# Kernel tuning notes

Hardware: AMD Instinct MI355X
Metric: run time of the kernel (lower is better)

The kernel has to match this reference:

```python
import jax, jax.numpy as jnp
import numpy as np

B, S, H, D, HID = 1024, 64, 32, 32, 1024
COMP = 256          # smolgen compress_size
TOK = 32            # smolgen token_compress out dim
LN_EPS = 1e-5


def _xavier(key, shape):
    fan_in, fan_out = shape[0], shape[-1]
    std = np.sqrt(2.0 / (fan_in + fan_out))
    return jax.random.normal(key, shape, dtype=jnp.float32) * std


def setup_inputs() -> dict:
    key = jax.random.key(0)
    ks = jax.random.split(key, 12)
    x = jax.random.normal(ks[0], (B, S, HID), dtype=jnp.float32)
    # attention projections (stored [in, out], no bias on qkv)
    Wq = _xavier(ks[1], (HID, H * D))
    Wk = _xavier(ks[2], (HID, H * D))
    Wv = _xavier(ks[3], (HID, H * D))
    Wo = _xavier(ks[4], (H * D, HID))
    bo = jnp.zeros((HID,), dtype=jnp.float32)
    pos_bias = jnp.zeros((H, S, S), dtype=jnp.float32)
    # smolgen params
    tc_W = _xavier(ks[5], (HID, TOK))                  # token_compress, no bias
    pc_W = _xavier(ks[6], (S * TOK, COMP))             # position_compress linear
    pc_b = jnp.zeros((COMP,), dtype=jnp.float32)
    ln_g = jnp.ones((COMP,), dtype=jnp.float32)        # LayerNorm gamma
    ln_b = jnp.zeros((COMP,), dtype=jnp.float32)       # LayerNorm beta
    hp_W = jax.vmap(lambda k: _xavier(k, (COMP, COMP)))(jax.random.split(ks[7], H))  # [H,COMP,COMP]
    hp_b = jnp.zeros((H, COMP), dtype=jnp.float32)
    alp_W = _xavier(ks[8], (COMP, S * S))              # attention_logits_proj
    alp_b = jnp.zeros((S * S,), dtype=jnp.float32)
    return dict(x=x, Wq=Wq, Wk=Wk, Wv=Wv, Wo=Wo, bo=bo, pos_bias=pos_bias,
                tc_W=tc_W, pc_W=pc_W, pc_b=pc_b, ln_g=ln_g, ln_b=ln_b,
                hp_W=hp_W, hp_b=hp_b, alp_W=alp_W, alp_b=alp_b)


def _smolgen(x, tc_W, pc_W, pc_b, ln_g, ln_b, hp_W, hp_b, alp_W, alp_b):
    b = x.shape[0]
    flat = (x @ tc_W).reshape(b, S * TOK)              # [B, 64*32]
    pv = jax.nn.relu(flat @ pc_W + pc_b)               # [B, COMP]
    mu = jnp.mean(pv, axis=-1, keepdims=True)
    var = jnp.mean(jnp.square(pv - mu), axis=-1, keepdims=True)
    pv = (pv - mu) * jax.lax.rsqrt(var + LN_EPS) * ln_g + ln_b
    # per-head projections, vectorized over heads
    hv = jnp.einsum('bc,hcd->bhd', pv, hp_W) + hp_b    # [B, H, COMP]
    logits = jnp.einsum('bhd,de->bhe', hv, alp_W) + alp_b
    return logits.reshape(b, H, S, S)


def reference(x, Wq, Wk, Wv, Wo, bo, pos_bias, tc_W, pc_W, pc_b, ln_g, ln_b,
              hp_W, hp_b, alp_W, alp_b):
    b = x.shape[0]
    scale = 1.0 / np.sqrt(D)
    q = (x @ Wq).reshape(b, S, H, D).transpose(0, 2, 1, 3)  # [B,H,S,D]
    k = (x @ Wk).reshape(b, S, H, D).transpose(0, 2, 1, 3)
    v = (x @ Wv).reshape(b, S, H, D).transpose(0, 2, 1, 3)
    scores = jnp.einsum('bhqd,bhkd->bhqk', q, k) * scale
    scores = scores + pos_bias[None]
    scores = scores + _smolgen(x, tc_W, pc_W, pc_b, ln_g, ln_b, hp_W, hp_b, alp_W, alp_b)
    attn = jax.nn.softmax(scores, axis=-1)
    out = jnp.einsum('bhqk,bhkd->bhqd', attn, v)             # [B,H,S,D]
    out = out.transpose(0, 2, 1, 3).reshape(b, S, H * D)
    return out @ Wo + bo
```

## Files before the change

### kernel.cpp

```cpp
#include <hip/hip_runtime.h>
#include <hip/hip_bf16.h>
#include <cstdint>
#include <cstddef>

typedef __attribute__((ext_vector_type(4))) float f32x4;
typedef __attribute__((ext_vector_type(8))) short short8;
typedef unsigned short u16;
typedef __attribute__((ext_vector_type(8))) unsigned short u16x8;
typedef __attribute__((ext_vector_type(4))) unsigned short u16x4;

__device__ __forceinline__ u16 f2bf(float f) {
  union { float f; unsigned u; } v; v.f = f;
  unsigned r = v.u + 0x7FFFu + ((v.u >> 16) & 1u);
  return (u16)(r >> 16);
}
__device__ __forceinline__ float bf2f(u16 h) {
  union { unsigned u; float f; } v; v.u = ((unsigned)h) << 16;
  return v.f;
}
__device__ __forceinline__ void gload16(const u16* g, const u16* l) {
  __builtin_amdgcn_global_load_lds((const __attribute__((address_space(1))) void*)g,
                                   (__attribute__((address_space(3))) void*)l, 16, 0, 0);
}
__device__ __forceinline__ void fenced_barrier() {
  __builtin_amdgcn_sched_barrier(0);
  __builtin_amdgcn_s_barrier();
  __builtin_amdgcn_sched_barrier(0);
}

__global__ __launch_bounds__(256) void prep_w2t(
    const float* __restrict__ Wq, const float* __restrict__ Wk, const float* __restrict__ Wv,
    const float* __restrict__ tc, u16* __restrict__ W2t)
{
  __shared__ float t[32][33];
  const int tx = threadIdx.x, ty = threadIdx.y;
  const int k0 = blockIdx.x * 32, n0 = blockIdx.y * 32;
  const float* src = nullptr; int col = 0, sw = 0;
  if      (n0 < 1024) { src = Wq; col = n0;        sw = 1024; }
  else if (n0 < 2048) { src = Wk; col = n0 - 1024; sw = 1024; }
  else if (n0 < 3072) { src = Wv; col = n0 - 2048; sw = 1024; }
  else if (n0 < 3104) { src = tc; col = n0 - 3072; sw = 32;   }
  if (src) {
    #pragma unroll
    for (int r = 0; r < 4; r++) {
      int k = k0 + ty + r * 8;
      t[ty + r * 8][tx] = src[(size_t)k * sw + col + tx];
    }
  }
  __syncthreads();
  #pragma unroll
  for (int r = 0; r < 4; r++) {
    int n = n0 + ty + r * 8, k = k0 + tx;
    u16 v = src ? f2bf(t[tx][ty + r * 8]) : (u16)0;
    W2t[(size_t)n * 1024 + k] = v;
  }
}

__global__ __launch_bounds__(256) void transpose_bf(
    const float* __restrict__ src, u16* __restrict__ dst, int R, int C)
{
  __shared__ float t[32][33];
  const int tx = threadIdx.x, ty = threadIdx.y;
  const size_t zoff = (size_t)blockIdx.z * R * C;
  src += zoff; dst += zoff;
  const int c0 = blockIdx.x * 32, r0 = blockIdx.y * 32;
  #pragma unroll
  for (int r = 0; r < 4; r++)
    t[ty + r * 8][tx] = src[(size_t)(r0 + ty + r * 8) * C + c0 + tx];
  __syncthreads();
  #pragma unroll
  for (int r = 0; r < 4; r++)
    dst[(size_t)(c0 + ty + r * 8) * R + r0 + tx] = f2bf(t[tx][ty + r * 8]);
}

__global__ __launch_bounds__(256) void cvt_x(const float* __restrict__ x, u16* __restrict__ A2)
{
  size_t i = (size_t)blockIdx.x * 256 + threadIdx.x;
  f32x4 v = ((const f32x4*)x)[i];
  u16x4 o;
  #pragma unroll
  for (int j = 0; j < 4; j++) o[j] = f2bf(v[j]);
  ((u16x4*)A2)[i] = o;
}

template<int MODE>
__global__ __launch_bounds__(256, 2) void gemm_p(
    const u16* __restrict__ A, const u16* __restrict__ Bt, int K,
    void* __restrict__ o0, void* __restrict__ o1, void* __restrict__ o2, void* __restrict__ o3,
    const float* __restrict__ bias0, const float* __restrict__ bias1)
{
  __shared__ __align__(16) u16 lds[3][12288];
  const int tid = threadIdx.x;
  const int wid = tid >> 6, lane = tid & 63;
  const int wm = wid >> 1, wn = wid & 1;
  const int g = lane >> 4, l15 = lane & 15;

  const int GX = gridDim.x;
  const int nwg = GX * (int)gridDim.y;
  const int lin = (int)blockIdx.y * GX + (int)blockIdx.x;
  const int swz = (lin & 7) * (nwg >> 3) + (lin >> 3);
  const int bn = swz % GX, bm = swz / GX;

  const int lR = lane >> 3;
  const int logi = (lane & 7) ^ lR;
  const int shb = logi >> 2;
  const int sg = logi & 3;

  const u16* pA[4];
  #pragma unroll
  for (int i = 0; i < 4; i++)
    pA[i] = A + (size_t)(bm * 256 + shb * 128 + (wid * 4 + i) * 8 + lR) * K + sg * 8;
  const u16* pB[2];
  #pragma unroll
  for (int i = 0; i < 2; i++)
    pB[i] = Bt + (size_t)(bn * 128 + shb * 64 + (wid * 2 + i) * 8 + lR) * K + sg * 8;

  const int aRd = l15 * 64 + ((((wm << 2) | g) ^ (l15 & 7)) << 3);
  const int bRd = 8192 + l15 * 64 + ((((wn << 2) | g) ^ (l15 & 7)) << 3);

  f32x4 acc[8][4];
  #pragma unroll
  for (int i = 0; i < 8; i++)
    #pragma unroll
    for (int j = 0; j < 4; j++)
      #pragma unroll
      for (int r = 0; r < 4; r++) acc[i][j][r] = 0.f;

  const int NT = K >> 5;

#define STG_A(buf, kt) do {                                              \
    _Pragma("unroll")                                                    \
    for (int i_ = 0; i_ < 4; i_++)                                       \
      gload16(pA[i_] + (size_t)(kt) * 32, &lds[buf][(wid * 4 + i_) * 512]); } while (0)
#define STG_B(buf, kt) do {                                              \
    _Pragma("unroll")                                                    \
    for (int i_ = 0; i_ < 2; i_++)                                       \
      gload16(pB[i_] + (size_t)(kt) * 32, &lds[buf][8192 + (wid * 2 + i_) * 512]); } while (0)

  STG_A(0, 0); STG_B(0, 0);
  STG_A(1, 1); STG_B(1, 1);

  for (int t = 0; t < NT; t++) {
    const int rb = t % 3;
    const int wb = (t + 2) % 3;
    const bool more = (t + 2) < NT;

    if (t + 1 < NT) asm volatile("s_waitcnt vmcnt(6)" ::: "memory");
    else            asm volatile("s_waitcnt vmcnt(0)" ::: "memory");
    fenced_barrier();

    short8 af[8], bfr[4];
    #pragma unroll
    for (int f = 0; f < 4; f++) af[f] = *(const short8*)&lds[rb][aRd + f * 1024];
    #pragma unroll
    for (int n = 0; n < 4; n++) bfr[n] = *(const short8*)&lds[rb][bRd + n * 1024];
    if (more) STG_A(wb, t + 2);
    asm volatile("s_waitcnt lgkmcnt(0)" ::: "memory");
    __builtin_amdgcn_sched_barrier(0);
    __builtin_amdgcn_s_setprio(1);
    #pragma unroll
    for (int f = 0; f < 4; f++)
      #pragma unroll
      for (int n = 0; n < 4; n++)
        acc[f][n] = __builtin_amdgcn_mfma_f32_16x16x32_bf16(af[f], bfr[n], acc[f][n], 0, 0, 0);
    __builtin_amdgcn_s_setprio(0);

    #pragma unroll
    for (int f = 4; f < 8; f++) af[f] = *(const short8*)&lds[rb][aRd + f * 1024];
    if (more) STG_B(wb, t + 2);
    asm volatile("s_waitcnt lgkmcnt(0)" ::: "memory");
    __builtin_amdgcn_sched_barrier(0);
    __builtin_amdgcn_s_setprio(1);
    #pragma unroll
    for (int f = 4; f < 8; f++)
      #pragma unroll
      for (int n = 0; n < 4; n++)
        acc[f][n] = __builtin_amdgcn_mfma_f32_16x16x32_bf16(af[f], bfr[n], acc[f][n], 0, 0, 0);
    __builtin_amdgcn_s_setprio(0);
  }
#undef STG_A
#undef STG_B

  const int lr = lane >> 4, lc = lane & 15;
  #pragma unroll
  for (int fm = 0; fm < 8; fm++) {
    #pragma unroll
    for (int fn = 0; fn < 4; fn++) {
      #pragma unroll
      for (int r = 0; r < 4; r++) {
        int gm = bm * 256 + wm * 128 + fm * 16 + lr * 4 + r;
        int gn = bn * 128 + wn * 64 + fn * 16 + lc;
        float val = acc[fm][fn][r];
        if (MODE == 0) {
          int b = gm >> 6, s = gm & 63;
          if (gn < 3072) {
            int which = gn >> 10, hh = (gn >> 5) & 31, d = gn & 31;
            u16* dst = (which == 0) ? (u16*)o0 : (which == 1) ? (u16*)o1 : (u16*)o2;
            dst[(((size_t)b * 32 + hh) * 64 + s) * 32 + d] = f2bf(val);
          } else if (gn < 3104) {
            ((u16*)o3)[(size_t)b * 2048 + s * 32 + (gn - 3072)] = f2bf(val);
          }
        } else if (MODE == 3) {
          ((u16*)o0)[(size_t)gm * 4096 + gn] = f2bf(val + bias0[gn] + bias1[(gm & 31) * 4096 + gn]);
        } else {
          ((float*)o0)[(size_t)gm * 1024 + gn] = val + bias0[gn];
        }
      }
    }
  }
}

template<int MODE>
__global__ __launch_bounds__(256) void gemm_bt(
    const u16* __restrict__ A, const u16* __restrict__ Bt, int K,
    void* __restrict__ o0, const float* __restrict__ bias0)
{
  __shared__ __align__(16) u16 lA[128 * 32];
  __shared__ __align__(16) u16 lB[128 * 32];
  const int tid = threadIdx.x;
  const int wid = tid >> 6, lane = tid & 63;
  const int wm = wid >> 1, wn = wid & 1;
  const int bn = blockIdx.x, bm = blockIdx.y;
  if (MODE == 2) Bt += (size_t)blockIdx.z * 256 * 256;

  f32x4 acc[4][4];
  #pragma unroll
  for (int i = 0; i < 4; i++)
    #pragma unroll
    for (int j = 0; j < 4; j++)
      #pragma unroll
      for (int r = 0; r < 4; r++) acc[i][j][r] = 0.f;

  const u16* Arow = A + (size_t)(bm * 128) * K;
  const u16* Brow = Bt + (size_t)(bn * 128) * K;

  for (int k0 = 0; k0 < K; k0 += 32) {
    #pragma unroll
    for (int i = 0; i < 2; i++) {
      int c = wid * 128 + i * 64 + lane;
      int row = c >> 2, col = (c & 3) * 8;
      gload16(Arow + (size_t)row * K + k0 + col, &lA[(wid * 128 + i * 64) * 8]);
      gload16(Brow + (size_t)row * K + k0 + col, &lB[(wid * 128 + i * 64) * 8]);
    }
    __syncthreads();
    short8 af[4], bfr[4];
    #pragma unroll
    for (int f = 0; f < 4; f++) {
      af[f]  = *(const short8*)&lA[(wm * 64 + f * 16 + (lane & 15)) * 32 + (lane >> 4) * 8];
      bfr[f] = *(const short8*)&lB[(wn * 64 + f * 16 + (lane & 15)) * 32 + (lane >> 4) * 8];
    }
    #pragma unroll
    for (int fm = 0; fm < 4; fm++)
      #pragma unroll
      for (int fn = 0; fn < 4; fn++)
        acc[fm][fn] = __builtin_amdgcn_mfma_f32_16x16x32_bf16(af[fm], bfr[fn], acc[fm][fn], 0, 0, 0);
    __syncthreads();
  }

  const int lr = lane >> 4, lc = lane & 15;
  #pragma unroll
  for (int fm = 0; fm < 4; fm++) {
    #pragma unroll
    for (int fn = 0; fn < 4; fn++) {
      #pragma unroll
      for (int r = 0; r < 4; r++) {
        int gm = bm * 128 + wm * 64 + fm * 16 + lr * 4 + r;
        int gn = bn * 128 + wn * 64 + fn * 16 + lc;
        float val = acc[fm][fn][r];
        if (MODE == 1) {
          float v = val + bias0[gn];
          ((float*)o0)[(size_t)gm * 256 + gn] = v > 0.f ? v : 0.f;
        } else if (MODE == 2) {
          int h = blockIdx.z;
          ((u16*)o0)[((size_t)gm * 32 + h) * 256 + gn] = f2bf(val + bias0[h * 256 + gn]);
        }
      }
    }
  }
}

__global__ __launch_bounds__(256) void ln_kernel(
    const float* __restrict__ pv, const float* __restrict__ g, const float* __restrict__ b2,
    u16* __restrict__ out)
{
  __shared__ float red[256];
  const int bi = blockIdx.x, t = threadIdx.x;
  float v = pv[(size_t)bi * 256 + t];
  red[t] = v; __syncthreads();
  #pragma unroll
  for (int o = 128; o > 0; o >>= 1) { if (t < o) red[t] += red[t + o]; __syncthreads(); }
  float mu = red[0] * (1.f / 256.f);
  __syncthreads();
  float dv = v - mu;
  red[t] = dv * dv; __syncthreads();
  #pragma unroll
  for (int o = 128; o > 0; o >>= 1) { if (t < o) red[t] += red[t + o]; __syncthreads(); }
  float var = red[0] * (1.f / 256.f);
  float rs = rsqrtf(var + 1e-5f);
  out[(size_t)bi * 256 + t] = f2bf(dv * rs * g[t] + b2[t]);
}

__global__ __launch_bounds__(64) void attn_mfma(
    const u16* __restrict__ qb, const u16* __restrict__ kb, const u16* __restrict__ vb,
    const u16* __restrict__ lg, u16* __restrict__ aout)
{
  __shared__ __align__(16) u16 vT[32 * 64];
  __shared__ __align__(16) u16 Pl[64 * 64];
  const int bid = blockIdx.x;
  const int lane = threadIdx.x;
  const int g = lane >> 4, l15 = lane & 15;
  const size_t base = (size_t)bid * 2048;

  {
    const u16* vrow = vb + base + lane * 32;
    u16x8 vv[4];
    #pragma unroll
    for (int c = 0; c < 4; c++) vv[c] = *(const u16x8*)(vrow + c * 8);
    #pragma unroll
    for (int d = 0; d < 32; d++)
      vT[d * 64 + (lane ^ ((d & 7) << 3))] = vv[d >> 3][d & 7];
  }

  short8 qf[4], kf[4];
  #pragma unroll
  for (int t = 0; t < 4; t++) {
    qf[t] = *(const short8*)(qb + base + (size_t)(t * 16 + l15) * 32 + g * 8);
    kf[t] = *(const short8*)(kb + base + (size_t)(t * 16 + l15) * 32 + g * 8);
  }

  f32x4 s[4][4];
  #pragma unroll
  for (int tm = 0; tm < 4; tm++)
    #pragma unroll
    for (int tn = 0; tn < 4; tn++)
      #pragma unroll
      for (int r = 0; r < 4; r++) s[tm][tn][r] = 0.f;
  #pragma unroll
  for (int tm = 0; tm < 4; tm++)
    #pragma unroll
    for (int tn = 0; tn < 4; tn++)
      s[tm][tn] = __builtin_amdgcn_mfma_f32_16x16x32_bf16(kf[tm], qf[tn], s[tm][tn], 0, 0, 0);

  const float scale = 0.17677669529663687f;
  float inv4[4];
  const u16* lbase = lg + (size_t)bid * 4096;
  #pragma unroll
  for (int tn = 0; tn < 4; tn++) {
    const int q = tn * 16 + l15;
    float mx = -1e30f;
    #pragma unroll
    for (int tm = 0; tm < 4; tm++) {
      u16x4 u = *(const u16x4*)(lbase + (size_t)q * 64 + tm * 16 + g * 4);
      #pragma unroll
      for (int r = 0; r < 4; r++) {
        s[tm][tn][r] = s[tm][tn][r] * scale + bf2f(u[r]);
        mx = fmaxf(mx, s[tm][tn][r]);
      }
    }
    mx = fmaxf(mx, __shfl_xor(mx, 16));
    mx = fmaxf(mx, __shfl_xor(mx, 32));
    float sm = 0.f;
    #pragma unroll
    for (int tm = 0; tm < 4; tm++)
      #pragma unroll
      for (int r = 0; r < 4; r++) {
        float e = __expf(s[tm][tn][r] - mx);
        s[tm][tn][r] = e;
        sm += e;
      }
    sm += __shfl_xor(sm, 16);
    sm += __shfl_xor(sm, 32);
    inv4[tn] = 1.f / sm;
    #pragma unroll
    for (int tm = 0; tm < 4; tm++) {
      u16x4 p;
      #pragma unroll
      for (int r = 0; r < 4; r++) p[r] = f2bf(s[tm][tn][r]);
      *(u16x4*)&Pl[q * 64 + ((tm * 16 + g * 4) ^ ((q & 7) << 3))] = p;
    }
  }
  __syncthreads();

  f32x4 o[2][4];
  #pragma unroll
  for (int md = 0; md < 2; md++)
    #pragma unroll
    for (int tn = 0; tn < 4; tn++)
      #pragma unroll
      for (int r = 0; r < 4; r++) o[md][tn][r] = 0.f;
  #pragma unroll
  for (int ks = 0; ks < 2; ks++) {
    short8 vf2[2], pf[4];
    #pragma unroll
    for (int md = 0; md < 2; md++)
      vf2[md] = *(const short8*)&vT[(md * 16 + l15) * 64 + ((ks * 32 + g * 8) ^ ((l15 & 7) << 3))];
    #pragma unroll
    for (int tn = 0; tn < 4; tn++)
      pf[tn] = *(const short8*)&Pl[(tn * 16 + l15) * 64 + ((ks * 32 + g * 8) ^ ((l15 & 7) << 3))];
    #pragma unroll
    for (int md = 0; md < 2; md++)
      #pragma unroll
      for (int tn = 0; tn < 4; tn++)
        o[md][tn] = __builtin_amdgcn_mfma_f32_16x16x32_bf16(vf2[md], pf[tn], o[md][tn], 0, 0, 0);
  }

  const int b = bid >> 5, h = bid & 31;
  #pragma unroll
  for (int md = 0; md < 2; md++) {
    #pragma unroll
    for (int tn = 0; tn < 4; tn++) {
      const int q = tn * 16 + l15, d0 = md * 16 + g * 4;
      u16x4 u;
      #pragma unroll
      for (int r = 0; r < 4; r++) u[r] = f2bf(o[md][tn][r] * inv4[tn]);
      *(u16x4*)(aout + ((size_t)(b * 64 + q)) * 1024 + h * 32 + d0) = u;
    }
  }
}

extern "C" void kernel_launch(void* const* d_in, const int* in_sizes, int n_in,
                              void* d_out, int out_size, void* d_ws, size_t ws_size,
                              hipStream_t stream) {
  const float* x       = (const float*)d_in[0];
  const float* Wq      = (const float*)d_in[1];
  const float* Wk      = (const float*)d_in[2];
  const float* Wv      = (const float*)d_in[3];
  const float* Wo      = (const float*)d_in[4];
  const float* bo      = (const float*)d_in[5];
  const float* pos_b   = (const float*)d_in[6];
  const float* tc_W    = (const float*)d_in[7];
  const float* pc_W    = (const float*)d_in[8];
  const float* pc_b    = (const float*)d_in[9];
  const float* ln_g    = (const float*)d_in[10];
  const float* ln_b    = (const float*)d_in[11];
  const float* hp_W    = (const float*)d_in[12];
  const float* hp_b    = (const float*)d_in[13];
  const float* alp_W   = (const float*)d_in[14];
  const float* alp_b   = (const float*)d_in[15];
  float* out = (float*)d_out;

  char* w = (char*)d_ws;
  u16* A2     = (u16*)w;
  u16* logits = (u16*)w;              w += 268435456;
  u16* qb     = (u16*)w;              w += 134217728;
  u16* kb     = (u16*)w;              w += 134217728;
  u16* vb     = (u16*)w;              w += 134217728;
  u16* aout   = (u16*)w;              w += 134217728;
  u16* W2t    = (u16*)w;              w += (size_t)3328 * 1024 * 2;
  u16* pcWt   = (u16*)w;              w += (size_t)256 * 2048 * 2;
  u16* hpWt   = (u16*)w;              w += (size_t)32 * 256 * 256 * 2;
  u16* alpWt  = (u16*)w;              w += (size_t)4096 * 256 * 2;
  u16* WoT    = (u16*)w;              w += (size_t)1024 * 1024 * 2;
  u16* flatb  = (u16*)w;              w += (size_t)1024 * 2048 * 2;
  float* pvtmp= (float*)w;            w += (size_t)1024 * 256 * 4;
  u16* pvb    = (u16*)w;              w += (size_t)1024 * 256 * 2;
  u16* hvb    = (u16*)w;              w += (size_t)32768 * 256 * 2;

  prep_w2t    <<<dim3(32, 104),    dim3(32, 8), 0, stream>>>(Wq, Wk, Wv, tc_W, W2t);
  transpose_bf<<<dim3(8, 64, 1),   dim3(32, 8), 0, stream>>>(pc_W, pcWt, 2048, 256);
  transpose_bf<<<dim3(8, 8, 32),   dim3(32, 8), 0, stream>>>(hp_W, hpWt, 256, 256);
  transpose_bf<<<dim3(128, 8, 1),  dim3(32, 8), 0, stream>>>(alp_W, alpWt, 256, 4096);
  transpose_bf<<<dim3(32, 32, 1),  dim3(32, 8), 0, stream>>>(Wo, WoT, 1024, 1024);
  cvt_x       <<<65536, 256, 0, stream>>>(x, A2);

  gemm_p<0> <<<dim3(26, 256),    256, 0, stream>>>(A2, W2t, 1024, qb, kb, vb, flatb, nullptr, nullptr);
  gemm_bt<1><<<dim3(2, 8),       256, 0, stream>>>(flatb, pcWt, 2048, pvtmp, pc_b);
  ln_kernel <<<1024, 256, 0, stream>>>(pvtmp, ln_g, ln_b, pvb);
  gemm_bt<2><<<dim3(2, 8, 32),   256, 0, stream>>>(pvb, hpWt, 256, hvb, hp_b);
  gemm_p<3> <<<dim3(32, 128),    256, 0, stream>>>(hvb, alpWt, 256, logits, nullptr, nullptr, nullptr, alp_b, pos_b);
  attn_mfma <<<32768, 64, 0, stream>>>(qb, kb, vb, logits, aout);
  gemm_p<4> <<<dim3(8, 256),     256, 0, stream>>>(aout, WoT, 1024, out, nullptr, nullptr, nullptr, bo, nullptr);
}
```

Before: 1.085 ms.

## Split gemm_p tile across 8 waves with 512 threads per block

The 256x128 GEMM tile is now computed by 8 waves (512 threads) instead of 4. Each wave owns a 64x64 sub-tile with a 4x4 accumulator array instead of 8x4. Staging drops to three global-to-LDS loads per thread, and the per-iteration work becomes a single MFMA phase. The aim is lower register pressure and more resident waves to hide latency, at the cost of less MFMA work per wave between barriers and more barrier participants.

```diff
diff --git a/kernel.cpp b/kernel.cpp
--- a/kernel.cpp
+++ b/kernel.cpp
@@ -84,7 +84,7 @@
 }
 
 template<int MODE>
-__global__ __launch_bounds__(256, 2) void gemm_p(
+__global__ __launch_bounds__(512, 4) void gemm_p(
     const u16* __restrict__ A, const u16* __restrict__ Bt, int K,
     void* __restrict__ o0, void* __restrict__ o1, void* __restrict__ o2, void* __restrict__ o3,
     const float* __restrict__ bias0, const float* __restrict__ bias1)
@@ -106,21 +106,16 @@
   const int shb = logi >> 2;
   const int sg = logi & 3;
 
-  const u16* pA[4];
+  const u16* pA0 = A + (size_t)(bm * 256 + shb * 128 + (wid * 2 + 0) * 8 + lR) * K + sg * 8;
+  const u16* pA1 = A + (size_t)(bm * 256 + shb * 128 + (wid * 2 + 1) * 8 + lR) * K + sg * 8;
+  const u16* pB  = Bt + (size_t)(bn * 128 + shb * 64 + wid * 8 + lR) * K + sg * 8;
+
+  const int aRd = ((wm & 1) * 64 + l15) * 64 + ((((wm >> 1) << 2) | g) ^ (l15 & 7)) * 8;
+  const int bRd = 8192 + l15 * 64 + ((((wn << 2) | g) ^ (l15 & 7)) * 8);
+
+  f32x4 acc[4][4];
   #pragma unroll
   for (int i = 0; i < 4; i++)
-    pA[i] = A + (size_t)(bm * 256 + shb * 128 + (wid * 4 + i) * 8 + lR) * K + sg * 8;
-  const u16* pB[2];
-  #pragma unroll
-  for (int i = 0; i < 2; i++)
-    pB[i] = Bt + (size_t)(bn * 128 + shb * 64 + (wid * 2 + i) * 8 + lR) * K + sg * 8;
-
-  const int aRd = l15 * 64 + ((((wm << 2) | g) ^ (l15 & 7)) << 3);
-  const int bRd = 8192 + l15 * 64 + ((((wn << 2) | g) ^ (l15 & 7)) << 3);
-
-  f32x4 acc[8][4];
-  #pragma unroll
-  for (int i = 0; i < 8; i++)
     #pragma unroll
     for (int j = 0; j < 4; j++)
       #pragma unroll
@@ -128,33 +123,28 @@
 
   const int NT = K >> 5;
 
-#define STG_A(buf, kt) do {                                              \
-    _Pragma("unroll")                                                    \
-    for (int i_ = 0; i_ < 4; i_++)                                       \
-      gload16(pA[i_] + (size_t)(kt) * 32, &lds[buf][(wid * 4 + i_) * 512]); } while (0)
-#define STG_B(buf, kt) do {                                              \
-    _Pragma("unroll")                                                    \
-    for (int i_ = 0; i_ < 2; i_++)                                       \
-      gload16(pB[i_] + (size_t)(kt) * 32, &lds[buf][8192 + (wid * 2 + i_) * 512]); } while (0)
-
-  STG_A(0, 0); STG_B(0, 0);
-  STG_A(1, 1); STG_B(1, 1);
+#define STG(buf, kt) do {                                                   \
+    gload16(pA0 + (size_t)(kt) * 32, &lds[buf][(wid * 2 + 0) * 512]);       \
+    gload16(pA1 + (size_t)(kt) * 32, &lds[buf][(wid * 2 + 1) * 512]);       \
+    gload16(pB  + (size_t)(kt) * 32, &lds[buf][8192 + wid * 512]); } while (0)
+
+  STG(0, 0); STG(1, 1);
 
   for (int t = 0; t < NT; t++) {
     const int rb = t % 3;
     const int wb = (t + 2) % 3;
     const bool more = (t + 2) < NT;
 
-    if (t + 1 < NT) asm volatile("s_waitcnt vmcnt(6)" ::: "memory");
+    if (t + 1 < NT) asm volatile("s_waitcnt vmcnt(3)" ::: "memory");
     else            asm volatile("s_waitcnt vmcnt(0)" ::: "memory");
     fenced_barrier();
 
-    short8 af[8], bfr[4];
+    short8 af[4], bfr[4];
     #pragma unroll
     for (int f = 0; f < 4; f++) af[f] = *(const short8*)&lds[rb][aRd + f * 1024];
     #pragma unroll
     for (int n = 0; n < 4; n++) bfr[n] = *(const short8*)&lds[rb][bRd + n * 1024];
-    if (more) STG_A(wb, t + 2);
+    if (more) STG(wb, t + 2);
     asm volatile("s_waitcnt lgkmcnt(0)" ::: "memory");
     __builtin_amdgcn_sched_barrier(0);
     __builtin_amdgcn_s_setprio(1);
@@ -164,31 +154,17 @@
       for (int n = 0; n < 4; n++)
         acc[f][n] = __builtin_amdgcn_mfma_f32_16x16x32_bf16(af[f], bfr[n], acc[f][n], 0, 0, 0);
     __builtin_amdgcn_s_setprio(0);
-
-    #pragma unroll
-    for (int f = 4; f < 8; f++) af[f] = *(const short8*)&lds[rb][aRd + f * 1024];
-    if (more) STG_B(wb, t + 2);
-    asm volatile("s_waitcnt lgkmcnt(0)" ::: "memory");
-    __builtin_amdgcn_sched_barrier(0);
-    __builtin_amdgcn_s_setprio(1);
-    #pragma unroll
-    for (int f = 4; f < 8; f++)
-      #pragma unroll
-      for (int n = 0; n < 4; n++)
-        acc[f][n] = __builtin_amdgcn_mfma_f32_16x16x32_bf16(af[f], bfr[n], acc[f][n], 0, 0, 0);
-    __builtin_amdgcn_s_setprio(0);
-  }
-#undef STG_A
-#undef STG_B
+  }
+#undef STG
 
   const int lr = lane >> 4, lc = lane & 15;
   #pragma unroll
-  for (int fm = 0; fm < 8; fm++) {
+  for (int fm = 0; fm < 4; fm++) {
     #pragma unroll
     for (int fn = 0; fn < 4; fn++) {
       #pragma unroll
       for (int r = 0; r < 4; r++) {
-        int gm = bm * 256 + wm * 128 + fm * 16 + lr * 4 + r;
+        int gm = bm * 256 + wm * 64 + fm * 16 + lr * 4 + r;
         int gn = bn * 128 + wn * 64 + fn * 16 + lc;
         float val = acc[fm][fn][r];
         if (MODE == 0) {
@@ -463,11 +439,11 @@
   transpose_bf<<<dim3(32, 32, 1),  dim3(32, 8), 0, stream>>>(Wo, WoT, 1024, 1024);
   cvt_x       <<<65536, 256, 0, stream>>>(x, A2);
 
-  gemm_p<0> <<<dim3(26, 256),    256, 0, stream>>>(A2, W2t, 1024, qb, kb, vb, flatb, nullptr, nullptr);
+  gemm_p<0> <<<dim3(26, 256),    512, 0, stream>>>(A2, W2t, 1024, qb, kb, vb, flatb, nullptr, nullptr);
   gemm_bt<1><<<dim3(2, 8),       256, 0, stream>>>(flatb, pcWt, 2048, pvtmp, pc_b);
   ln_kernel <<<1024, 256, 0, stream>>>(pvtmp, ln_g, ln_b, pvb);
   gemm_bt<2><<<dim3(2, 8, 32),   256, 0, stream>>>(pvb, hpWt, 256, hvb, hp_b);
-  gemm_p<3> <<<dim3(32, 128),    256, 0, stream>>>(hvb, alpWt, 256, logits, nullptr, nullptr, nullptr, alp_b, pos_b);
+  gemm_p<3> <<<dim3(32, 128),    512, 0, stream>>>(hvb, alpWt, 256, logits, nullptr, nullptr, nullptr, alp_b, pos_b);
   attn_mfma <<<32768, 64, 0, stream>>>(qb, kb, vb, logits, aout);
-  gemm_p<4> <<<dim3(8, 256),     256, 0, stream>>>(aout, WoT, 1024, out, nullptr, nullptr, nullptr, bo, nullptr);
-}
+  gemm_p<4> <<<dim3(8, 256),     512, 0, stream>>>(aout, WoT, 1024, out, nullptr, nullptr, nullptr, bo, nullptr);
+}
```

Result: no change. 1.089 ms (+0.3%).
